# Optimization experiments

Measured on AMD Instinct MI355X. Metric: run time of the kernel, lower is better.

The kernel has to match this reference:

```python
import jax, jax.numpy as jnp
import numpy as np

B, C_IN, C_OUT, H, W, K, NK = 16, 256, 256, 64, 64, 3, 2
EPS = 1e-8


def setup_inputs() -> dict:
    key = jax.random.key(0)
    k1, k2, k3, k4 = jax.random.split(key, 4)
    x = jax.random.normal(k1, (B, C_IN, H, W), dtype=jnp.float32)
    mod = jax.random.normal(k2, (B, C_IN), dtype=jnp.float32)
    kernel_mod = jax.random.normal(k3, (B, NK), dtype=jnp.float32)
    # kernel bank: [num_conv_kernels, dim_out, dim_in, k, k] (kaiming-ish scale)
    weights = jax.random.normal(k4, (NK, C_OUT, C_IN, K, K), dtype=jnp.float32) / np.sqrt(C_IN * K * K)
    gamma = jnp.ones((C_OUT,), dtype=jnp.float32)
    return {"x": x, "mod": mod, "kernel_mod": kernel_mod, "weights": weights, "gamma": gamma}


def _block(x, mod, kernel_mod, weights, gamma):
    # adaptive kernel selection: softmax-mix the kernel bank per sample
    attn = jax.nn.softmax(kernel_mod, axis=-1)                       # [b, n]
    w = jnp.einsum('bn,noikl->boikl', attn, weights)                 # [b, o, i, k, k]
    # style modulation over input channels
    w = w * (mod[:, None, :, None, None] + 1.0)
    # demodulation
    denom = jnp.clip(jnp.sum(w * w, axis=(2, 3, 4), keepdims=True), EPS)
    w = w * jax.lax.rsqrt(denom)
    # per-sample conv (groups=b trick in torch) -> vmap over batch
    def conv_one(fmap, wb):
        return jax.lax.conv_general_dilated(
            fmap[None], wb, window_strides=(1, 1), padding='SAME',
            dimension_numbers=('NCHW', 'OIHW', 'NCHW'))[0]
    y = jax.vmap(conv_one)(x, w)                                     # [b, o, h, w]
    # RMSNorm over channel dim: F.normalize(x, dim=1) * gamma * sqrt(dim)
    norm = jnp.sqrt(jnp.sum(y * y, axis=1, keepdims=True))
    y = y / jnp.maximum(norm, 1e-12)
    y = y * gamma[None, :, None, None] * (gamma.shape[0] ** 0.5)
    # SiLU
    return y * jax.nn.sigmoid(y)


def reference(x, mod, kernel_mod, weights, gamma):
    return _block(x, mod, kernel_mod, weights, gamma)
```

## Files before the change

kernel.cpp:

```cpp
#include <hip/hip_runtime.h>
#include <math.h>


typedef __attribute__((ext_vector_type(8))) short short8;
typedef __attribute__((ext_vector_type(16))) float f32x16;

#define GLL16(src, dst)                                                       \
  __builtin_amdgcn_global_load_lds(                                           \
      (const __attribute__((address_space(1))) unsigned int*)(src),           \
      (__attribute__((address_space(3))) unsigned int*)(dst), 16, 0, 0)

static __device__ __forceinline__ unsigned short f2bf(float v) {
  union { float f; unsigned u; } u;
  u.f = v;
  unsigned r = u.u + 0x7FFF + ((u.u >> 16) & 1);
  return (unsigned short)(r >> 16);
}

__global__ __launch_bounds__(256) void prep_all(
    const float* __restrict__ x, const float* __restrict__ mod,
    const float* __restrict__ kmod, const float* __restrict__ weights,
    unsigned short* __restrict__ wq, unsigned short* __restrict__ xq) {
  __shared__ __align__(16) unsigned short xs2[1056];
  __shared__ float red[8][32];
  __shared__ float scl[8];
  int t = threadIdx.x;

  if (blockIdx.x < 16896) {
    int blk = blockIdx.x;
    int rowp = blk % 66;
    int bc = blk / 66;
    int b = bc >> 4, c = bc & 15;
    size_t obase = (size_t)blk * 1056;

    if (rowp == 0 || rowp == 65) {
      for (int idx = t; idx < 1056; idx += 256) xq[obase + idx] = 0;
      return;
    }
    int row = rowp - 1;
    for (int idx = t; idx < 1056; idx += 256) xs2[idx] = 0;
    __syncthreads();
#pragma unroll
    for (int k = 0; k < 4; ++k) {
      int idx = t + k * 256;
      int il = idx >> 6, col = idx & 63;
      float v = x[(((size_t)b * 256 + c * 16 + il) * 64 + row) * 64 + col];
      xs2[(col + 1) * 16 + il] = f2bf(v);
    }
    __syncthreads();
    if (t < 132) *(short8*)(xq + obase + (size_t)t * 8) = *(const short8*)&xs2[t * 8];
  } else {
    int blk = blockIdx.x - 16896;
    int b = blk >> 5, oq = blk & 31;
    int o_l = t >> 5, its = t & 31;
    int o = oq * 8 + o_l;

    float k0 = kmod[b * 2 + 0], k1 = kmod[b * 2 + 1];
    float mx = fmaxf(k0, k1);
    float e0 = expf(k0 - mx), e1 = expf(k1 - mx);
    float ai = 1.0f / (e0 + e1);
    float a0 = e0 * ai, a1 = e1 * ai;

    float wv[9][8];
    float s = 0.0f;
    const float* w0 = &weights[((size_t)o * 256 + its * 8) * 9];
    const float* w1 = w0 + 589824;
#pragma unroll
    for (int e = 0; e < 8; ++e) {
      float f = mod[b * 256 + its * 8 + e] + 1.0f;
#pragma unroll
      for (int j = 0; j < 9; ++j) {
        float v = (a0 * w0[e * 9 + j] + a1 * w1[e * 9 + j]) * f;
        wv[j][e] = v;
        s = fmaf(v, v, s);
      }
    }

    red[o_l][its] = s;
    __syncthreads();
    if (t < 8) {
      float tot = 0.0f;
#pragma unroll
      for (int k = 0; k < 32; ++k) tot += red[t][k];
      scl[t] = rsqrtf(fmaxf(tot, 1e-8f));
    }
    __syncthreads();
    float sc = scl[o_l];

    int c = its >> 1, io = its & 1;
    int oh = o >> 7, mf = (o >> 5) & 3;
    int lane2 = (o & 31) + io * 32;
    size_t cbase = ((size_t)(b * 16 + c)) * 36864 + oh * 2048 + mf * 512 + lane2 * 8;
#pragma unroll
    for (int j = 0; j < 9; ++j) {
      short8 pk;
#pragma unroll
      for (int e = 0; e < 8; ++e) pk[e] = (short)f2bf(wv[j][e] * sc);
      *(short8*)(wq + cbase + j * 4096) = pk;
    }
  }
}

__global__ __launch_bounds__(256, 2) void conv_fused(
    const unsigned short* __restrict__ xq, const unsigned short* __restrict__ wq,
    const float* __restrict__ gamma, float* __restrict__ out) {
  __shared__ __align__(16) unsigned short xsm[2][6144];
  __shared__ float redl[512];
  __shared__ float invs[128];
  __shared__ float gsm[256];

  int bid = blockIdx.x;
  int xcd = bid & 7;
  int kk = bid >> 3;
  int b = xcd * 2 + (kk >> 5);
  int rt = kk & 31;
  int r0 = rt * 2;

  int t = threadIdx.x;
  int w = t >> 6, lane = t & 63;
  int oh = w & 1, ps = w >> 1;
  int l31 = lane & 31, l5 = lane >> 5;

  gsm[t] = gamma[t];

  int boffs[9];
#pragma unroll
  for (int T = 0; T < 9; ++T) {
    int kh = T / 3, kw = T % 3;
    boffs[T] = (ps + kh) * 2112 + (l31 + kw) * 32 + l5 * 16;
  }

  f32x16 acc[4][2];
#pragma unroll
  for (int mf = 0; mf < 4; ++mf)
#pragma unroll
    for (int h = 0; h < 2; ++h)
#pragma unroll
      for (int q = 0; q < 16; ++q) acc[mf][h][q] = 0.f;

#define GLLX(cn, nb)                                                           \
  _Pragma("unroll") for (int r = 0; r < 3; ++r) {                              \
    GLL16(xq + ((size_t)((b * 16 + (cn)) * 66 + r0)) * 1056 + (r * 256 + t) * 8, \
          &xsm[nb][(r * 256 + t) * 8]);                                        \
  }

#define AGLB(SA, CC, TT)                                                       \
  {                                                                            \
    const unsigned short* ap_ = wq + (size_t)(b * 16 + (CC)) * 36864 +         \
                                (TT) * 4096 + oh * 2048 + lane * 8;            \
    _Pragma("unroll") for (int mf = 0; mf < 4; ++mf)                           \
        SA[mf] = *(const short8*)(ap_ + mf * 512);                             \
  }

#define BDSRD(SB, T, XB)                                                       \
  {                                                                            \
    _Pragma("unroll") for (int h = 0; h < 2; ++h)                              \
        SB[h] = *(const short8*)((XB) + boffs[T] + h * 1024);                  \
  }

#define MFMA8(SA, SB)                                                          \
  {                                                                            \
    __builtin_amdgcn_s_setprio(1);                                             \
    _Pragma("unroll") for (int h = 0; h < 2; ++h)                              \
        _Pragma("unroll") for (int mf = 0; mf < 4; ++mf)                       \
            acc[mf][h] = __builtin_amdgcn_mfma_f32_32x32x16_bf16(              \
                SA[mf], SB[h], acc[mf][h], 0, 0, 0);                           \
    __builtin_amdgcn_s_setprio(0);                                             \
  }

#define SBAR __builtin_amdgcn_sched_barrier(0)
#define LGKM0 asm volatile("s_waitcnt lgkmcnt(0)" ::: "memory")
#define VMC(n) asm volatile("s_waitcnt vmcnt(" #n ")" ::: "memory")
#define BAR __builtin_amdgcn_s_barrier()

  short8 PA[4], QA[4], PB[2], QB[2];

  const char* xs0 = (const char*)xsm[0];
  const char* xs1 = (const char*)xsm[1];

#define STEP(C, A0, A1, XB, NB)                                                \
  {                                                                            \
    int CN = (C) < 15 ? (C) + 1 : 15;                                          \
    GLLX(CN, NB);                                                              \
    BDSRD(PB, 0, XB); SBAR;                                                    \
    BDSRD(QB, 1, XB); SBAR; MFMA8(A0, PB); AGLB(A0, (C), 2); SBAR;             \
    BDSRD(PB, 2, XB); SBAR; MFMA8(A1, QB); AGLB(A1, (C), 3); SBAR;             \
    BDSRD(QB, 3, XB); SBAR; MFMA8(A0, PB); AGLB(A0, (C), 4); SBAR;             \
    BDSRD(PB, 4, XB); SBAR; MFMA8(A1, QB); AGLB(A1, (C), 5); SBAR;             \
    BDSRD(QB, 5, XB); SBAR; MFMA8(A0, PB); AGLB(A0, (C), 6); SBAR;             \
    BDSRD(PB, 6, XB); SBAR; MFMA8(A1, QB); AGLB(A1, (C), 7); SBAR;             \
    BDSRD(QB, 7, XB); SBAR; MFMA8(A0, PB); AGLB(A0, (C), 8); SBAR;             \
    BDSRD(PB, 8, XB); SBAR; MFMA8(A1, QB); AGLB(A1, CN, 0); SBAR;              \
    MFMA8(A0, PB); AGLB(A0, CN, 1); SBAR;                                      \
    LGKM0;                                                                     \
    VMC(8);                                                                    \
    BAR;                                                                       \
    SBAR;                                                                      \
  }

  GLLX(0, 0);
  AGLB(PA, 0, 0);
  AGLB(QA, 0, 1);
  VMC(8);
  BAR;
  SBAR;

  for (int cc = 0; cc < 16; cc += 2) {
    STEP(cc, PA, QA, xs0, 1);
    STEP(cc + 1, QA, PA, xs1, 0);
  }

#pragma unroll
  for (int h = 0; h < 2; ++h) {
    float pssum = 0.f;
#pragma unroll
    for (int mf = 0; mf < 4; ++mf)
#pragma unroll
      for (int q = 0; q < 16; ++q) {
        float v = acc[mf][h][q];
        pssum = fmaf(v, v, pssum);
      }
    int px = ps * 64 + h * 32 + l31;
    redl[(oh * 2 + l5) * 128 + px] = pssum;
  }
  __syncthreads();
  if (t < 128) {
    float ssum = redl[t] + redl[128 + t] + redl[256 + t] + redl[384 + t];
    invs[t] = 16.0f / fmaxf(sqrtf(ssum), 1e-12f);
  }
  __syncthreads();
  float iv2[2];
#pragma unroll
  for (int h = 0; h < 2; ++h) iv2[h] = invs[ps * 64 + h * 32 + l31];

#pragma unroll
  for (int mf = 0; mf < 4; ++mf)
#pragma unroll
    for (int q = 0; q < 16; ++q) {
      int o = oh * 128 + mf * 32 + (q & 3) + 8 * (q >> 2) + 4 * l5;
      float g = gsm[o];
      size_t ob = ((size_t)b * 256 + o) * 64 + (r0 + ps);
#pragma unroll
      for (int h = 0; h < 2; ++h) {
        float v = acc[mf][h][q] * iv2[h] * g;
        float sg = 1.0f / (1.0f + expf(-v));
        out[ob * 64 + h * 32 + l31] = v * sg;
      }
    }
#undef GLLX
#undef AGLB
#undef BDSRD
#undef MFMA8
#undef SBAR
#undef LGKM0
#undef VMC
#undef BAR
#undef STEP
}

extern "C" void kernel_launch(void* const* d_in, const int* in_sizes, int n_in,
                              void* d_out, int out_size, void* d_ws, size_t ws_size,
                              hipStream_t stream) {
  const float* x = (const float*)d_in[0];
  const float* mod = (const float*)d_in[1];
  const float* kmod = (const float*)d_in[2];
  const float* weights = (const float*)d_in[3];
  const float* gamma = (const float*)d_in[4];
  float* out = (float*)d_out;

  unsigned short* xq = (unsigned short*)d_ws;
  unsigned short* wq = (unsigned short*)((char*)d_ws + 35684352);

  prep_all<<<16896 + 512, 256, 0, stream>>>(x, mod, kmod, weights, wq, xq);
  conv_fused<<<512, 256, 0, stream>>>(xq, wq, gamma, out);
}
```

Before: 130.6 us.

## Triple-buffer weight register prefetch in conv loop and split prep kernel

```diff
diff --git a/kernel.cpp b/kernel.cpp
--- a/kernel.cpp
+++ b/kernel.cpp
@@ -17,88 +17,88 @@
   return (unsigned short)(r >> 16);
 }
 
-__global__ __launch_bounds__(256) void prep_all(
-    const float* __restrict__ x, const float* __restrict__ mod,
-    const float* __restrict__ kmod, const float* __restrict__ weights,
-    unsigned short* __restrict__ wq, unsigned short* __restrict__ xq) {
-  __shared__ __align__(16) unsigned short xs2[1056];
+__global__ __launch_bounds__(256) void wprep(
+    const float* __restrict__ mod, const float* __restrict__ kmod,
+    const float* __restrict__ weights, unsigned short* __restrict__ wq) {
+  int blk = blockIdx.x;
+  int b = blk >> 5, oq = blk & 31;
+  int t = threadIdx.x;
+  int o_l = t >> 5, its = t & 31;
+  int o = oq * 8 + o_l;
+
+  float k0 = kmod[b * 2 + 0], k1 = kmod[b * 2 + 1];
+  float mx = fmaxf(k0, k1);
+  float e0 = expf(k0 - mx), e1 = expf(k1 - mx);
+  float ai = 1.0f / (e0 + e1);
+  float a0 = e0 * ai, a1 = e1 * ai;
+
+  float wv[9][8];
+  float s = 0.0f;
+  const float* w0 = &weights[((size_t)o * 256 + its * 8) * 9];
+  const float* w1 = w0 + 589824;
+#pragma unroll
+  for (int e = 0; e < 8; ++e) {
+    float f = mod[b * 256 + its * 8 + e] + 1.0f;
+#pragma unroll
+    for (int j = 0; j < 9; ++j) {
+      float v = (a0 * w0[e * 9 + j] + a1 * w1[e * 9 + j]) * f;
+      wv[j][e] = v;
+      s = fmaf(v, v, s);
+    }
+  }
+
   __shared__ float red[8][32];
   __shared__ float scl[8];
+  red[o_l][its] = s;
+  __syncthreads();
+  if (t < 8) {
+    float tot = 0.0f;
+#pragma unroll
+    for (int k = 0; k < 32; ++k) tot += red[t][k];
+    scl[t] = rsqrtf(fmaxf(tot, 1e-8f));
+  }
+  __syncthreads();
+  float sc = scl[o_l];
+
+  int c = its >> 1, io = its & 1;
+  int oh = o >> 7, mf = (o >> 5) & 3;
+  int lane2 = (o & 31) + io * 32;
+  size_t cbase = ((size_t)(b * 16 + c)) * 36864 + oh * 2048 + mf * 512 + lane2 * 8;
+#pragma unroll
+  for (int j = 0; j < 9; ++j) {
+    short8 pk;
+#pragma unroll
+    for (int e = 0; e < 8; ++e) pk[e] = (short)f2bf(wv[j][e] * sc);
+    *(short8*)(wq + cbase + j * 4096) = pk;
+  }
+}
+
+__global__ __launch_bounds__(256) void xprep(
+    const float* __restrict__ x, unsigned short* __restrict__ xq) {
+  int blk = blockIdx.x;
+  int rowp = blk % 66;
+  int bc = blk / 66;
+  int b = bc >> 4, c = bc & 15;
   int t = threadIdx.x;
-
-  if (blockIdx.x < 16896) {
-    int blk = blockIdx.x;
-    int rowp = blk % 66;
-    int bc = blk / 66;
-    int b = bc >> 4, c = bc & 15;
-    size_t obase = (size_t)blk * 1056;
-
-    if (rowp == 0 || rowp == 65) {
-      for (int idx = t; idx < 1056; idx += 256) xq[obase + idx] = 0;
-      return;
-    }
-    int row = rowp - 1;
-    for (int idx = t; idx < 1056; idx += 256) xs2[idx] = 0;
-    __syncthreads();
-#pragma unroll
-    for (int k = 0; k < 4; ++k) {
-      int idx = t + k * 256;
-      int il = idx >> 6, col = idx & 63;
-      float v = x[(((size_t)b * 256 + c * 16 + il) * 64 + row) * 64 + col];
-      xs2[(col + 1) * 16 + il] = f2bf(v);
-    }
-    __syncthreads();
-    if (t < 132) *(short8*)(xq + obase + (size_t)t * 8) = *(const short8*)&xs2[t * 8];
-  } else {
-    int blk = blockIdx.x - 16896;
-    int b = blk >> 5, oq = blk & 31;
-    int o_l = t >> 5, its = t & 31;
-    int o = oq * 8 + o_l;
-
-    float k0 = kmod[b * 2 + 0], k1 = kmod[b * 2 + 1];
-    float mx = fmaxf(k0, k1);
-    float e0 = expf(k0 - mx), e1 = expf(k1 - mx);
-    float ai = 1.0f / (e0 + e1);
-    float a0 = e0 * ai, a1 = e1 * ai;
-
-    float wv[9][8];
-    float s = 0.0f;
-    const float* w0 = &weights[((size_t)o * 256 + its * 8) * 9];
-    const float* w1 = w0 + 589824;
-#pragma unroll
-    for (int e = 0; e < 8; ++e) {
-      float f = mod[b * 256 + its * 8 + e] + 1.0f;
-#pragma unroll
-      for (int j = 0; j < 9; ++j) {
-        float v = (a0 * w0[e * 9 + j] + a1 * w1[e * 9 + j]) * f;
-        wv[j][e] = v;
-        s = fmaf(v, v, s);
-      }
-    }
-
-    red[o_l][its] = s;
-    __syncthreads();
-    if (t < 8) {
-      float tot = 0.0f;
-#pragma unroll
-      for (int k = 0; k < 32; ++k) tot += red[t][k];
-      scl[t] = rsqrtf(fmaxf(tot, 1e-8f));
-    }
-    __syncthreads();
-    float sc = scl[o_l];
-
-    int c = its >> 1, io = its & 1;
-    int oh = o >> 7, mf = (o >> 5) & 3;
-    int lane2 = (o & 31) + io * 32;
-    size_t cbase = ((size_t)(b * 16 + c)) * 36864 + oh * 2048 + mf * 512 + lane2 * 8;
-#pragma unroll
-    for (int j = 0; j < 9; ++j) {
-      short8 pk;
-#pragma unroll
-      for (int e = 0; e < 8; ++e) pk[e] = (short)f2bf(wv[j][e] * sc);
-      *(short8*)(wq + cbase + j * 4096) = pk;
-    }
-  }
+  size_t obase = (size_t)blk * 1056;
+
+  if (rowp == 0 || rowp == 65) {
+    for (int idx = t; idx < 1056; idx += 256) xq[obase + idx] = 0;
+    return;
+  }
+  __shared__ __align__(16) unsigned short xs2[1056];
+  int row = rowp - 1;
+  for (int idx = t; idx < 1056; idx += 256) xs2[idx] = 0;
+  __syncthreads();
+#pragma unroll
+  for (int k = 0; k < 4; ++k) {
+    int idx = t + k * 256;
+    int il = idx >> 6, col = idx & 63;
+    float v = x[(((size_t)b * 256 + c * 16 + il) * 64 + row) * 64 + col];
+    xs2[(col + 1) * 16 + il] = f2bf(v);
+  }
+  __syncthreads();
+  if (t < 132) *(short8*)(xq + obase + (size_t)t * 8) = *(const short8*)&xs2[t * 8];
 }
 
 __global__ __launch_bounds__(256, 2) void conv_fused(
@@ -173,41 +173,38 @@
 #define VMC(n) asm volatile("s_waitcnt vmcnt(" #n ")" ::: "memory")
 #define BAR __builtin_amdgcn_s_barrier()
 
-  short8 PA[4], QA[4], PB[2], QB[2];
+  short8 S0[4], S1[4], S2[4], PB[2], QB[2];
 
   const char* xs0 = (const char*)xsm[0];
   const char* xs1 = (const char*)xsm[1];
 
-#define STEP(C, A0, A1, XB, NB)                                                \
-  {                                                                            \
-    int CN = (C) < 15 ? (C) + 1 : 15;                                          \
-    GLLX(CN, NB);                                                              \
-    BDSRD(PB, 0, XB); SBAR;                                                    \
-    BDSRD(QB, 1, XB); SBAR; MFMA8(A0, PB); AGLB(A0, (C), 2); SBAR;             \
-    BDSRD(PB, 2, XB); SBAR; MFMA8(A1, QB); AGLB(A1, (C), 3); SBAR;             \
-    BDSRD(QB, 3, XB); SBAR; MFMA8(A0, PB); AGLB(A0, (C), 4); SBAR;             \
-    BDSRD(PB, 4, XB); SBAR; MFMA8(A1, QB); AGLB(A1, (C), 5); SBAR;             \
-    BDSRD(QB, 5, XB); SBAR; MFMA8(A0, PB); AGLB(A0, (C), 6); SBAR;             \
-    BDSRD(PB, 6, XB); SBAR; MFMA8(A1, QB); AGLB(A1, (C), 7); SBAR;             \
-    BDSRD(QB, 7, XB); SBAR; MFMA8(A0, PB); AGLB(A0, (C), 8); SBAR;             \
-    BDSRD(PB, 8, XB); SBAR; MFMA8(A1, QB); AGLB(A1, CN, 0); SBAR;              \
-    MFMA8(A0, PB); AGLB(A0, CN, 1); SBAR;                                      \
-    LGKM0;                                                                     \
-    VMC(8);                                                                    \
-    BAR;                                                                       \
-    SBAR;                                                                      \
-  }
-
   GLLX(0, 0);
-  AGLB(PA, 0, 0);
-  AGLB(QA, 0, 1);
-  VMC(8);
+  AGLB(S0, 0, 0);
+  AGLB(S1, 0, 1);
+  AGLB(S2, 0, 2);
+  VMC(12);
   BAR;
   SBAR;
 
-  for (int cc = 0; cc < 16; cc += 2) {
-    STEP(cc, PA, QA, xs0, 1);
-    STEP(cc + 1, QA, PA, xs1, 0);
+  for (int c = 0; c < 16; ++c) {
+    const char* XB = (c & 1) ? xs1 : xs0;
+    int NB = (c & 1) ^ 1;
+    int CN = c < 15 ? c + 1 : 15;
+    GLLX(CN, NB);
+    BDSRD(PB, 0, XB); SBAR;
+    BDSRD(QB, 1, XB); SBAR; MFMA8(S0, PB); AGLB(S0, c, 3); SBAR;
+    BDSRD(PB, 2, XB); SBAR; MFMA8(S1, QB); AGLB(S1, c, 4); SBAR;
+    BDSRD(QB, 3, XB); SBAR; MFMA8(S2, PB); AGLB(S2, c, 5); SBAR;
+    BDSRD(PB, 4, XB); SBAR; MFMA8(S0, QB); AGLB(S0, c, 6); SBAR;
+    BDSRD(QB, 5, XB); SBAR; MFMA8(S1, PB); AGLB(S1, c, 7); SBAR;
+    BDSRD(PB, 6, XB); SBAR; MFMA8(S2, QB); AGLB(S2, c, 8); SBAR;
+    BDSRD(QB, 7, XB); SBAR; MFMA8(S0, PB); AGLB(S0, CN, 0); SBAR;
+    BDSRD(PB, 8, XB); SBAR; MFMA8(S1, QB); AGLB(S1, CN, 1); SBAR;
+    MFMA8(S2, PB); AGLB(S2, CN, 2); SBAR;
+    LGKM0;
+    VMC(12);
+    BAR;
+    SBAR;
   }
 
 #pragma unroll
@@ -255,7 +252,6 @@
 #undef LGKM0
 #undef VMC
 #undef BAR
-#undef STEP
 }
 
 extern "C" void kernel_launch(void* const* d_in, const int* in_sizes, int n_in,
@@ -271,6 +267,7 @@
   unsigned short* xq = (unsigned short*)d_ws;
   unsigned short* wq = (unsigned short*)((char*)d_ws + 35684352);
 
-  prep_all<<<16896 + 512, 256, 0, stream>>>(x, mod, kmod, weights, wq, xq);
+  wprep<<<512, 256, 0, stream>>>(mod, kmod, weights, wq);
+  xprep<<<16 * 16 * 66, 256, 0, stream>>>(x, xq);
   conv_fused<<<512, 256, 0, stream>>>(xq, wq, gamma, out);
 }
```

Result: faster. 122.5 us (-6.2%).
